# Optimization experiments

Measured on AMD Instinct MI355X. Metric: run time of the kernel, lower is better.

Reference implementation:

```python
import jax, jax.numpy as jnp
import numpy as np

N, K, DIM = 100000, 16, 128


def setup_inputs() -> dict:
    key = jax.random.key(0)
    k1, k2, k3, k4 = jax.random.split(key, 4)
    latents = jax.random.normal(k1, (N, DIM), dtype=jnp.float32)
    neighbors = jax.random.randint(k2, (N, K), 0, N, dtype=jnp.int64)
    # score MLP params: Linear(2*dim -> dim), ReLU, Linear(dim -> 1)
    s1 = 1.0 / np.sqrt(2 * DIM)
    s2 = 1.0 / np.sqrt(DIM)
    W1 = jax.random.uniform(k3, (2 * DIM, DIM), minval=-s1, maxval=s1, dtype=jnp.float32)
    b1 = jnp.zeros((DIM,), dtype=jnp.float32)
    W2 = jax.random.uniform(k4, (DIM, 1), minval=-s2, maxval=s2, dtype=jnp.float32)
    b2 = jnp.zeros((1,), dtype=jnp.float32)
    return {"latents": latents, "neighbors": neighbors, "W1": W1, "b1": b1, "W2": W2, "b2": b2}


def reference(latents, neighbors, W1, b1, W2, b2):
    # latents: [N, D]; neighbors: [N, K] int indices
    nbr = latents[neighbors]                                  # [N, K, D] gather
    central = jnp.broadcast_to(latents[:, None, :], nbr.shape)  # [N, K, D]
    pair = jnp.concatenate([central, nbr], axis=-1)           # [N, K, 2D]
    h = jax.nn.relu(jnp.einsum('nkd,dh->nkh', pair, W1) + b1)  # [N, K, D]
    scores = (jnp.einsum('nkh,ho->nko', h, W2) + b2)[..., 0]   # [N, K]
    weights = jax.nn.softmax(scores, axis=-1)                  # [N, K]
    return jnp.einsum('nk,nkd->nd', weights, nbr)              # [N, D]
```

## Files before the change

kernel.cpp:

```cpp
#include <hip/hip_runtime.h>
#include <hip/hip_bf16.h>

#define DIM 128
#define KNB 16

using fragAB = __attribute__((ext_vector_type(8))) short;
using f32x4  = __attribute__((ext_vector_type(4))) float;
using u32x4  = __attribute__((ext_vector_type(4))) unsigned int;

union frag_u { fragAB s; u32x4 u; };

__device__ __forceinline__ unsigned short bf16bits(float f) {
    union { float f; unsigned u; } v; v.f = f;
    unsigned r = v.u + 0x7fffu + ((v.u >> 16) & 1u);
    return (unsigned short)(r >> 16);
}
__device__ __forceinline__ unsigned cvt_pk_bf16(float lo, float hi) {
    unsigned r;
    asm("v_cvt_pk_bf16_f32 %0, %1, %2" : "=v"(r) : "v"(lo), "v"(hi));
    return r;
}
__device__ __forceinline__ float bflo(unsigned u) { return __uint_as_float(u << 16); }
__device__ __forceinline__ float bfhi(unsigned u) { return __uint_as_float(u & 0xffff0000u); }

__global__ __launch_bounds__(256) void na_w1t(
    const float* __restrict__ W1, const float* __restrict__ W2,
    unsigned short* __restrict__ W1T, unsigned short* __restrict__ W2b)
{
    int idx = blockIdx.x * 256 + threadIdx.x;
    int hp = idx >> 7, d = idx & 127;
    float v = (hp < DIM) ? W1[(size_t)d * DIM + hp]
                         : W1[(size_t)(DIM + d) * DIM + (hp - DIM)];
    W1T[idx] = bf16bits(v);
    if (blockIdx.x == 0 && threadIdx.x < DIM) W2b[threadIdx.x] = bf16bits(W2[threadIdx.x]);
}

__global__ __launch_bounds__(256) void na_precompute_mfma(
    const float* __restrict__ lat, const unsigned short* __restrict__ W1T,
    const float* __restrict__ b1, unsigned short* __restrict__ Ab,
    unsigned short* __restrict__ P, int nNodes)
{
    __shared__ unsigned char w1lds[256 * 256];

    const int wave = threadIdx.x >> 6;
    const int lane = threadIdx.x & 63;
    const int lg = lane >> 4, lr = lane & 15;
    const int mbase = blockIdx.x * 128 + wave * 32;

#pragma unroll
    for (int p = 0; p < 16; ++p) {
        int g = p * 256 + threadIdx.x;
        int row = g >> 4, c = g & 15;
        u32x4 v = *(const u32x4*)(W1T + (size_t)g * 8);
        *(u32x4*)(w1lds + row * 256 + ((c * 16) ^ ((row & 7) << 4))) = v;
    }

    f32x4 acc0[16], acc1[16];
#pragma unroll
    for (int i = 0; i < 16; ++i) {
        acc0[i] = (f32x4){0.f, 0.f, 0.f, 0.f};
        acc1[i] = (f32x4){0.f, 0.f, 0.f, 0.f};
    }

    const int r0 = mbase + lr;
    const int r1 = mbase + 16 + lr;
    const bool v0 = r0 < nNodes, v1 = r1 < nNodes;
    const float* p0 = lat + (size_t)(v0 ? r0 : (nNodes - 1)) * DIM;
    const float* p1 = lat + (size_t)(v1 ? r1 : (nNodes - 1)) * DIM;

    frag_u bl0[4], bl1[4];
#pragma unroll
    for (int ks = 0; ks < 4; ++ks) {
        f32x4 lo0 = *(const f32x4*)(p0 + ks * 32 + lg * 8);
        f32x4 hi0 = *(const f32x4*)(p0 + ks * 32 + lg * 8 + 4);
        f32x4 lo1 = *(const f32x4*)(p1 + ks * 32 + lg * 8);
        f32x4 hi1 = *(const f32x4*)(p1 + ks * 32 + lg * 8 + 4);
        bl0[ks].u[0] = cvt_pk_bf16(lo0[0], lo0[1]);
        bl0[ks].u[1] = cvt_pk_bf16(lo0[2], lo0[3]);
        bl0[ks].u[2] = cvt_pk_bf16(hi0[0], hi0[1]);
        bl0[ks].u[3] = cvt_pk_bf16(hi0[2], hi0[3]);
        bl1[ks].u[0] = cvt_pk_bf16(lo1[0], lo1[1]);
        bl1[ks].u[1] = cvt_pk_bf16(lo1[2], lo1[3]);
        bl1[ks].u[2] = cvt_pk_bf16(hi1[0], hi1[1]);
        bl1[ks].u[3] = cvt_pk_bf16(hi1[2], hi1[3]);
    }

    __syncthreads();

    const unsigned char* wbase = w1lds + lr * 256;
    const int xm = (lr & 7) << 4;
#pragma unroll
    for (int ks = 0; ks < 4; ++ks) {
        const int co = (ks * 64) | (lg * 16);
        const unsigned char* wk = wbase + (co ^ xm);
#pragma unroll
        for (int nt = 0; nt < 16; ++nt) {
            fragAB af = *(const fragAB*)(wk + nt * 4096);
            acc0[nt] = __builtin_amdgcn_mfma_f32_16x16x32_bf16(af, bl0[ks].s, acc0[nt], 0, 0, 0);
            acc1[nt] = __builtin_amdgcn_mfma_f32_16x16x32_bf16(af, bl1[ks].s, acc1[nt], 0, 0, 0);
        }
    }

    if (v0) {
        unsigned short* arow = Ab + (size_t)r0 * DIM;
        unsigned short* prow = P  + (size_t)r0 * 256;
#pragma unroll
        for (int nt = 0; nt < 8; ++nt) {
            float4 bv = *(const float4*)(b1 + nt * 16 + lg * 4);
            uint2 pk;
            pk.x = cvt_pk_bf16(acc0[nt][0] + bv.x, acc0[nt][1] + bv.y);
            pk.y = cvt_pk_bf16(acc0[nt][2] + bv.z, acc0[nt][3] + bv.w);
            *(uint2*)(arow + nt * 16 + lg * 4) = pk;
        }
#pragma unroll
        for (int nt = 8; nt < 16; ++nt) {
            uint2 pk;
            pk.x = cvt_pk_bf16(acc0[nt][0], acc0[nt][1]);
            pk.y = cvt_pk_bf16(acc0[nt][2], acc0[nt][3]);
            *(uint2*)(prow + (nt - 8) * 16 + lg * 4) = pk;
        }
#pragma unroll
        for (int ks = 0; ks < 4; ++ks)
            *(fragAB*)(prow + DIM + ks * 32 + lg * 8) = bl0[ks].s;
    }
    if (v1) {
        unsigned short* arow = Ab + (size_t)r1 * DIM;
        unsigned short* prow = P  + (size_t)r1 * 256;
#pragma unroll
        for (int nt = 0; nt < 8; ++nt) {
            float4 bv = *(const float4*)(b1 + nt * 16 + lg * 4);
            uint2 pk;
            pk.x = cvt_pk_bf16(acc1[nt][0] + bv.x, acc1[nt][1] + bv.y);
            pk.y = cvt_pk_bf16(acc1[nt][2] + bv.z, acc1[nt][3] + bv.w);
            *(uint2*)(arow + nt * 16 + lg * 4) = pk;
        }
#pragma unroll
        for (int nt = 8; nt < 16; ++nt) {
            uint2 pk;
            pk.x = cvt_pk_bf16(acc1[nt][0], acc1[nt][1]);
            pk.y = cvt_pk_bf16(acc1[nt][2], acc1[nt][3]);
            *(uint2*)(prow + (nt - 8) * 16 + lg * 4) = pk;
        }
#pragma unroll
        for (int ks = 0; ks < 4; ++ks)
            *(fragAB*)(prow + DIM + ks * 32 + lg * 8) = bl1[ks].s;
    }
}

__global__ __launch_bounds__(256) void na_score_agg(
    const int* __restrict__ nbr, const unsigned short* __restrict__ Ab,
    const unsigned short* __restrict__ Pu, const unsigned int* __restrict__ P32,
    const unsigned short* __restrict__ W2b, float* __restrict__ out, int nNodes)
{
    const int wave = threadIdx.x >> 6;
    const int lane = threadIdx.x & 63;
    const int lg = lane >> 4, lr = lane & 15;
    const int n = blockIdx.x * 4 + wave;
    if (n >= nNodes) return;

    const int jl = nbr[n * KNB + lr];

    frag_u fB[4];
    const unsigned short* Pj = Pu + (size_t)jl * 256;
#pragma unroll
    for (int ks = 0; ks < 4; ++ks)
        fB[ks].s = *(const fragAB*)(Pj + ks * 32 + lg * 8);

    unsigned bL[KNB];
#pragma unroll
    for (int k = 0; k < KNB; ++k) {
        int j = __shfl(jl, k);
        bL[k] = P32[(size_t)j * 128 + 64 + lane];
    }

    frag_u fA[4]; fragAB fW[4];
    const unsigned short* An = Ab + (size_t)n * DIM;
#pragma unroll
    for (int ks = 0; ks < 4; ++ks) {
        fA[ks].s = *(const fragAB*)(An + ks * 32 + lg * 8);
        fW[ks]   = *(const fragAB*)(W2b + ks * 32 + lg * 8);
    }

    f32x4 accS = (f32x4){0.f, 0.f, 0.f, 0.f};
#pragma unroll
    for (int ks = 0; ks < 4; ++ks) {
        u32x4 alo = fA[ks].u << 16, ahi = fA[ks].u & 0xffff0000u;
        u32x4 blo = fB[ks].u << 16, bhi = fB[ks].u & 0xffff0000u;
        frag_u h;
#pragma unroll
        for (int p = 0; p < 4; ++p) {
            float h0 = fmaxf(__uint_as_float(alo[p]) + __uint_as_float(blo[p]), 0.f);
            float h1 = fmaxf(__uint_as_float(ahi[p]) + __uint_as_float(bhi[p]), 0.f);
            h.u[p] = cvt_pk_bf16(h0, h1);
        }
        accS = __builtin_amdgcn_mfma_f32_16x16x32_bf16(h.s, fW[ks], accS, 0, 0, 0);
    }

    float m = fmaxf(fmaxf(accS[0], accS[1]), fmaxf(accS[2], accS[3]));
    m = fmaxf(m, __shfl_xor(m, 16));
    m = fmaxf(m, __shfl_xor(m, 32));

    float e4[4];
#pragma unroll
    for (int r = 0; r < 4; ++r) e4[r] = __expf(accS[r] - m);

    float sum = e4[0] + e4[1] + e4[2] + e4[3];
    sum += __shfl_xor(sum, 16);
    sum += __shfl_xor(sum, 32);
    const float inv = 1.f / sum;

    const bool hi1 = lg & 1, hi2 = lg & 2;
    float o4[4];
#pragma unroll
    for (int r = 0; r < 4; ++r) o4[r] = __shfl_xor(e4[r], 16);
    float v8[8];
#pragma unroll
    for (int r = 0; r < 4; ++r) {
        v8[r]     = hi1 ? o4[r] : e4[r];
        v8[4 + r] = hi1 ? e4[r] : o4[r];
    }
    float o8[8];
#pragma unroll
    for (int i = 0; i < 8; ++i) o8[i] = __shfl_xor(v8[i], 32);
    float e[KNB];
#pragma unroll
    for (int i = 0; i < 8; ++i) {
        e[i]     = hi2 ? o8[i] : v8[i];
        e[8 + i] = hi2 ? v8[i] : o8[i];
    }

    float o0 = 0.f, o1 = 0.f;
#pragma unroll
    for (int k = 0; k < KNB; ++k) {
        o0 += e[k] * bflo(bL[k]);
        o1 += e[k] * bfhi(bL[k]);
    }

    float2 o; o.x = o0 * inv; o.y = o1 * inv;
    *(float2*)(out + (size_t)n * DIM + 2 * lane) = o;
}

__global__ __launch_bounds__(256) void na_naive(
    const float* __restrict__ lat, const int* __restrict__ nbr,
    const float* __restrict__ W1, const float* __restrict__ b1,
    const float* __restrict__ W2, float* __restrict__ out, int nNodes)
{
    const int wave = threadIdx.x >> 6;
    const int lane = threadIdx.x & 63;
    const int n = blockIdx.x * 4 + wave;
    if (n >= nNodes) return;

    const int d0 = lane, d1 = lane + 64;
    const float w20 = W2[d0];
    const float w21 = W2[d1];
    const float c0 = lat[(size_t)n * DIM + d0];
    const float c1 = lat[(size_t)n * DIM + d1];

    float a0 = b1[d0], a1 = b1[d1];
    for (int r = 0; r < DIM; ++r) {
        float cv = (r < 64) ? __shfl(c0, r) : __shfl(c1, r - 64);
        a0 += cv * W1[(size_t)r * DIM + d0];
        a1 += cv * W1[(size_t)r * DIM + d1];
    }

    const int jl = nbr[n * KNB + (lane & 15)];
    float s[KNB], nl0[KNB], nl1[KNB];

    for (int k = 0; k < KNB; ++k) {
        int j = __shfl(jl, k);
        float l0 = lat[(size_t)j * DIM + d0];
        float l1 = lat[(size_t)j * DIM + d1];
        nl0[k] = l0; nl1[k] = l1;
        float h0 = a0, h1 = a1;
        for (int r = 0; r < DIM; ++r) {
            float nv = (r < 64) ? __shfl(l0, r) : __shfl(l1, r - 64);
            h0 += nv * W1[(size_t)(DIM + r) * DIM + d0];
            h1 += nv * W1[(size_t)(DIM + r) * DIM + d1];
        }
        h0 = fmaxf(h0, 0.f);
        h1 = fmaxf(h1, 0.f);
        float p = h0 * w20 + h1 * w21;
#pragma unroll
        for (int off = 32; off; off >>= 1) p += __shfl_xor(p, off);
        s[k] = p;
    }

    float m = s[0];
#pragma unroll
    for (int k = 1; k < KNB; ++k) m = fmaxf(m, s[k]);
    float sum = 0.f;
#pragma unroll
    for (int k = 0; k < KNB; ++k) { s[k] = expf(s[k] - m); sum += s[k]; }
    float inv = 1.f / sum;

    float o0 = 0.f, o1 = 0.f;
#pragma unroll
    for (int k = 0; k < KNB; ++k) { o0 += s[k] * nl0[k]; o1 += s[k] * nl1[k]; }

    out[(size_t)n * DIM + d0] = o0 * inv;
    out[(size_t)n * DIM + d1] = o1 * inv;
}

extern "C" void kernel_launch(void* const* d_in, const int* in_sizes, int n_in,
                              void* d_out, int out_size, void* d_ws, size_t ws_size,
                              hipStream_t stream)
{
    const float* lat = (const float*)d_in[0];
    const int*   nbr = (const int*)  d_in[1];
    const float* W1  = (const float*)d_in[2];
    const float* b1  = (const float*)d_in[3];
    const float* W2  = (const float*)d_in[4];
    float* out = (float*)d_out;

    const int nNodes = in_sizes[0] / DIM;
    const size_t bytesAb = (size_t)nNodes * DIM * sizeof(unsigned short);
    const size_t bytesP  = (size_t)nNodes * 256 * sizeof(unsigned short);
    const size_t bytesW  = (256 * DIM + DIM) * sizeof(unsigned short);

    if (ws_size >= bytesAb + bytesP + bytesW) {
        unsigned short* Ab  = (unsigned short*)d_ws;
        unsigned short* P   = (unsigned short*)((char*)d_ws + bytesAb);
        unsigned short* W1T = (unsigned short*)((char*)d_ws + bytesAb + bytesP);
        unsigned short* W2b = W1T + 256 * DIM;
        na_w1t<<<128, 256, 0, stream>>>(W1, W2, W1T, W2b);
        na_precompute_mfma<<<(nNodes + 127) / 128, 256, 0, stream>>>(lat, W1T, b1, Ab, P, nNodes);
        na_score_agg<<<(nNodes + 3) / 4, 256, 0, stream>>>(nbr, Ab, P, (const unsigned int*)P, W2b, out, nNodes);
    } else {
        na_naive<<<(nNodes + 3) / 4, 256, 0, stream>>>(lat, nbr, W1, b1, W2, out, nNodes);
    }
}
```

Measured before the change: 162.3 us.

## Recompute neighbor projection per edge via MFMA instead of storing per-node P

The precompute kernel now computes and stores only the central-node projection (with bias) and a bf16 copy of latents, no longer the neighbor projection half of W1. The score kernel loads the neighbor half of W1 into LDS and recomputes each neighbor's projection per edge with MFMA, fusing ReLU and the W2 dot into the epilogue. It processes two nodes per wave in a persistent grid-stride loop. This trades far less precompute writing and a smaller gathered row for 16x more matmul work in the score kernel.

```diff
diff --git a/kernel.cpp b/kernel.cpp
--- a/kernel.cpp
+++ b/kernel.cpp
@@ -38,9 +38,9 @@
 __global__ __launch_bounds__(256) void na_precompute_mfma(
     const float* __restrict__ lat, const unsigned short* __restrict__ W1T,
     const float* __restrict__ b1, unsigned short* __restrict__ Ab,
-    unsigned short* __restrict__ P, int nNodes)
-{
-    __shared__ unsigned char w1lds[256 * 256];
+    unsigned short* __restrict__ latb, int nNodes)
+{
+    __shared__ unsigned char w1lds[128 * 256];
 
     const int wave = threadIdx.x >> 6;
     const int lane = threadIdx.x & 63;
@@ -48,18 +48,11 @@
     const int mbase = blockIdx.x * 128 + wave * 32;
 
 #pragma unroll
-    for (int p = 0; p < 16; ++p) {
+    for (int p = 0; p < 8; ++p) {
         int g = p * 256 + threadIdx.x;
         int row = g >> 4, c = g & 15;
         u32x4 v = *(const u32x4*)(W1T + (size_t)g * 8);
         *(u32x4*)(w1lds + row * 256 + ((c * 16) ^ ((row & 7) << 4))) = v;
-    }
-
-    f32x4 acc0[16], acc1[16];
-#pragma unroll
-    for (int i = 0; i < 16; ++i) {
-        acc0[i] = (f32x4){0.f, 0.f, 0.f, 0.f};
-        acc1[i] = (f32x4){0.f, 0.f, 0.f, 0.f};
     }
 
     const int r0 = mbase + lr;
@@ -87,6 +80,13 @@
 
     __syncthreads();
 
+    f32x4 acc0[8], acc1[8];
+#pragma unroll
+    for (int i = 0; i < 8; ++i) {
+        acc0[i] = (f32x4){0.f, 0.f, 0.f, 0.f};
+        acc1[i] = (f32x4){0.f, 0.f, 0.f, 0.f};
+    }
+
     const unsigned char* wbase = w1lds + lr * 256;
     const int xm = (lr & 7) << 4;
 #pragma unroll
@@ -94,7 +94,7 @@
         const int co = (ks * 64) | (lg * 16);
         const unsigned char* wk = wbase + (co ^ xm);
 #pragma unroll
-        for (int nt = 0; nt < 16; ++nt) {
+        for (int nt = 0; nt < 8; ++nt) {
             fragAB af = *(const fragAB*)(wk + nt * 4096);
             acc0[nt] = __builtin_amdgcn_mfma_f32_16x16x32_bf16(af, bl0[ks].s, acc0[nt], 0, 0, 0);
             acc1[nt] = __builtin_amdgcn_mfma_f32_16x16x32_bf16(af, bl1[ks].s, acc1[nt], 0, 0, 0);
@@ -102,8 +102,8 @@
     }
 
     if (v0) {
-        unsigned short* arow = Ab + (size_t)r0 * DIM;
-        unsigned short* prow = P  + (size_t)r0 * 256;
+        unsigned short* arow = Ab   + (size_t)r0 * DIM;
+        unsigned short* lrow = latb + (size_t)r0 * DIM;
 #pragma unroll
         for (int nt = 0; nt < 8; ++nt) {
             float4 bv = *(const float4*)(b1 + nt * 16 + lg * 4);
@@ -113,19 +113,12 @@
             *(uint2*)(arow + nt * 16 + lg * 4) = pk;
         }
 #pragma unroll
-        for (int nt = 8; nt < 16; ++nt) {
-            uint2 pk;
-            pk.x = cvt_pk_bf16(acc0[nt][0], acc0[nt][1]);
-            pk.y = cvt_pk_bf16(acc0[nt][2], acc0[nt][3]);
-            *(uint2*)(prow + (nt - 8) * 16 + lg * 4) = pk;
-        }
-#pragma unroll
         for (int ks = 0; ks < 4; ++ks)
-            *(fragAB*)(prow + DIM + ks * 32 + lg * 8) = bl0[ks].s;
+            *(fragAB*)(lrow + ks * 32 + lg * 8) = bl0[ks].s;
     }
     if (v1) {
-        unsigned short* arow = Ab + (size_t)r1 * DIM;
-        unsigned short* prow = P  + (size_t)r1 * 256;
+        unsigned short* arow = Ab   + (size_t)r1 * DIM;
+        unsigned short* lrow = latb + (size_t)r1 * DIM;
 #pragma unroll
         for (int nt = 0; nt < 8; ++nt) {
             float4 bv = *(const float4*)(b1 + nt * 16 + lg * 4);
@@ -135,109 +128,121 @@
             *(uint2*)(arow + nt * 16 + lg * 4) = pk;
         }
 #pragma unroll
-        for (int nt = 8; nt < 16; ++nt) {
-            uint2 pk;
-            pk.x = cvt_pk_bf16(acc1[nt][0], acc1[nt][1]);
-            pk.y = cvt_pk_bf16(acc1[nt][2], acc1[nt][3]);
-            *(uint2*)(prow + (nt - 8) * 16 + lg * 4) = pk;
-        }
-#pragma unroll
         for (int ks = 0; ks < 4; ++ks)
-            *(fragAB*)(prow + DIM + ks * 32 + lg * 8) = bl1[ks].s;
+            *(fragAB*)(lrow + ks * 32 + lg * 8) = bl1[ks].s;
     }
 }
 
 __global__ __launch_bounds__(256) void na_score_agg(
     const int* __restrict__ nbr, const unsigned short* __restrict__ Ab,
-    const unsigned short* __restrict__ Pu, const unsigned int* __restrict__ P32,
-    const unsigned short* __restrict__ W2b, float* __restrict__ out, int nNodes)
-{
+    const unsigned short* __restrict__ latb, const unsigned int* __restrict__ latb32,
+    const unsigned short* __restrict__ W1T, const unsigned short* __restrict__ W2b,
+    float* __restrict__ out, int nNodes)
+{
+    __shared__ unsigned char w1lds[128 * 256];
+
     const int wave = threadIdx.x >> 6;
     const int lane = threadIdx.x & 63;
     const int lg = lane >> 4, lr = lane & 15;
-    const int n = blockIdx.x * 4 + wave;
-    if (n >= nNodes) return;
-
-    const int jl = nbr[n * KNB + lr];
-
-    frag_u fB[4];
-    const unsigned short* Pj = Pu + (size_t)jl * 256;
-#pragma unroll
-    for (int ks = 0; ks < 4; ++ks)
-        fB[ks].s = *(const fragAB*)(Pj + ks * 32 + lg * 8);
-
-    unsigned bL[KNB];
-#pragma unroll
-    for (int k = 0; k < KNB; ++k) {
-        int j = __shfl(jl, k);
-        bL[k] = P32[(size_t)j * 128 + 64 + lane];
-    }
-
-    frag_u fA[4]; fragAB fW[4];
-    const unsigned short* An = Ab + (size_t)n * DIM;
-#pragma unroll
-    for (int ks = 0; ks < 4; ++ks) {
-        fA[ks].s = *(const fragAB*)(An + ks * 32 + lg * 8);
-        fW[ks]   = *(const fragAB*)(W2b + ks * 32 + lg * 8);
-    }
-
-    f32x4 accS = (f32x4){0.f, 0.f, 0.f, 0.f};
-#pragma unroll
-    for (int ks = 0; ks < 4; ++ks) {
-        u32x4 alo = fA[ks].u << 16, ahi = fA[ks].u & 0xffff0000u;
-        u32x4 blo = fB[ks].u << 16, bhi = fB[ks].u & 0xffff0000u;
-        frag_u h;
-#pragma unroll
-        for (int p = 0; p < 4; ++p) {
-            float h0 = fmaxf(__uint_as_float(alo[p]) + __uint_as_float(blo[p]), 0.f);
-            float h1 = fmaxf(__uint_as_float(ahi[p]) + __uint_as_float(bhi[p]), 0.f);
-            h.u[p] = cvt_pk_bf16(h0, h1);
-        }
-        accS = __builtin_amdgcn_mfma_f32_16x16x32_bf16(h.s, fW[ks], accS, 0, 0, 0);
-    }
-
-    float m = fmaxf(fmaxf(accS[0], accS[1]), fmaxf(accS[2], accS[3]));
-    m = fmaxf(m, __shfl_xor(m, 16));
-    m = fmaxf(m, __shfl_xor(m, 32));
-
-    float e4[4];
-#pragma unroll
-    for (int r = 0; r < 4; ++r) e4[r] = __expf(accS[r] - m);
-
-    float sum = e4[0] + e4[1] + e4[2] + e4[3];
-    sum += __shfl_xor(sum, 16);
-    sum += __shfl_xor(sum, 32);
-    const float inv = 1.f / sum;
-
-    const bool hi1 = lg & 1, hi2 = lg & 2;
-    float o4[4];
-#pragma unroll
-    for (int r = 0; r < 4; ++r) o4[r] = __shfl_xor(e4[r], 16);
-    float v8[8];
-#pragma unroll
-    for (int r = 0; r < 4; ++r) {
-        v8[r]     = hi1 ? o4[r] : e4[r];
-        v8[4 + r] = hi1 ? e4[r] : o4[r];
-    }
-    float o8[8];
-#pragma unroll
-    for (int i = 0; i < 8; ++i) o8[i] = __shfl_xor(v8[i], 32);
-    float e[KNB];
-#pragma unroll
-    for (int i = 0; i < 8; ++i) {
-        e[i]     = hi2 ? o8[i] : v8[i];
-        e[8 + i] = hi2 ? v8[i] : o8[i];
-    }
-
-    float o0 = 0.f, o1 = 0.f;
-#pragma unroll
-    for (int k = 0; k < KNB; ++k) {
-        o0 += e[k] * bflo(bL[k]);
-        o1 += e[k] * bfhi(bL[k]);
-    }
-
-    float2 o; o.x = o0 * inv; o.y = o1 * inv;
-    *(float2*)(out + (size_t)n * DIM + 2 * lane) = o;
+
+#pragma unroll
+    for (int p = 0; p < 8; ++p) {
+        int g = p * 256 + threadIdx.x;
+        int row = g >> 4, c = g & 15;
+        u32x4 v = *(const u32x4*)(W1T + (size_t)(128 + row) * DIM + c * 8);
+        *(u32x4*)(w1lds + row * 256 + ((c * 16) ^ ((row & 7) << 4))) = v;
+    }
+    __syncthreads();
+
+    const unsigned char* wbase = w1lds + lr * 256;
+    const int xm = (lr & 7) << 4;
+    const int nPairs = (nNodes + 1) >> 1;
+
+    for (int pr = blockIdx.x * 4 + wave; pr < nPairs; pr += gridDim.x * 4) {
+        const int n0 = 2 * pr;
+        const int n1 = n0 + 1;
+        const bool has1 = n1 < nNodes;
+        const int n1c = has1 ? n1 : n0;
+
+        const int jl0 = nbr[n0  * KNB + lr];
+        const int jl1 = nbr[n1c * KNB + lr];
+
+        frag_u fL0[4], fL1[4];
+        const unsigned short* L0 = latb + (size_t)jl0 * DIM;
+        const unsigned short* L1 = latb + (size_t)jl1 * DIM;
+#pragma unroll
+        for (int ks = 0; ks < 4; ++ks) {
+            fL0[ks].s = *(const fragAB*)(L0 + ks * 32 + lg * 8);
+            fL1[ks].s = *(const fragAB*)(L1 + ks * 32 + lg * 8);
+        }
+
+        float sacc0 = 0.f, sacc1 = 0.f;
+        const unsigned short* An0 = Ab + (size_t)n0  * DIM;
+        const unsigned short* An1 = Ab + (size_t)n1c * DIM;
+#pragma unroll
+        for (int nt = 0; nt < 8; ++nt) {
+            f32x4 acc0 = (f32x4){0.f, 0.f, 0.f, 0.f};
+            f32x4 acc1 = (f32x4){0.f, 0.f, 0.f, 0.f};
+#pragma unroll
+            for (int ks = 0; ks < 4; ++ks) {
+                const int co = (ks * 64) | (lg * 16);
+                fragAB af = *(const fragAB*)(wbase + nt * 4096 + (co ^ xm));
+                acc0 = __builtin_amdgcn_mfma_f32_16x16x32_bf16(af, fL0[ks].s, acc0, 0, 0, 0);
+                acc1 = __builtin_amdgcn_mfma_f32_16x16x32_bf16(af, fL1[ks].s, acc1, 0, 0, 0);
+            }
+            uint2 a0 = *(const uint2*)(An0 + nt * 16 + lg * 4);
+            uint2 a1 = *(const uint2*)(An1 + nt * 16 + lg * 4);
+            uint2 wv = *(const uint2*)(W2b + nt * 16 + lg * 4);
+            float w0 = bflo(wv.x), w1 = bfhi(wv.x), w2 = bflo(wv.y), w3 = bfhi(wv.y);
+            sacc0 += fmaxf(bflo(a0.x) + acc0[0], 0.f) * w0
+                   + fmaxf(bfhi(a0.x) + acc0[1], 0.f) * w1
+                   + fmaxf(bflo(a0.y) + acc0[2], 0.f) * w2
+                   + fmaxf(bfhi(a0.y) + acc0[3], 0.f) * w3;
+            sacc1 += fmaxf(bflo(a1.x) + acc1[0], 0.f) * w0
+                   + fmaxf(bfhi(a1.x) + acc1[1], 0.f) * w1
+                   + fmaxf(bflo(a1.y) + acc1[2], 0.f) * w2
+                   + fmaxf(bfhi(a1.y) + acc1[3], 0.f) * w3;
+        }
+        float s0 = sacc0 + __shfl_xor(sacc0, 16);
+        s0 += __shfl_xor(s0, 32);
+        float s1 = sacc1 + __shfl_xor(sacc1, 16);
+        s1 += __shfl_xor(s1, 32);
+
+        float m0 = s0, m1 = s1;
+#pragma unroll
+        for (int off = 1; off < 16; off <<= 1) {
+            m0 = fmaxf(m0, __shfl_xor(m0, off));
+            m1 = fmaxf(m1, __shfl_xor(m1, off));
+        }
+        float e0 = __expf(s0 - m0);
+        float e1 = __expf(s1 - m1);
+        float sum0 = e0, sum1 = e1;
+#pragma unroll
+        for (int off = 1; off < 16; off <<= 1) {
+            sum0 += __shfl_xor(sum0, off);
+            sum1 += __shfl_xor(sum1, off);
+        }
+        const float inv0 = 1.f / sum0;
+        const float inv1 = 1.f / sum1;
+
+        float o00 = 0.f, o01 = 0.f, o10 = 0.f, o11 = 0.f;
+#pragma unroll
+        for (int k = 0; k < KNB; ++k) {
+            int j0 = __shfl(jl0, k); float ek0 = __shfl(e0, k);
+            int j1 = __shfl(jl1, k); float ek1 = __shfl(e1, k);
+            unsigned u0 = latb32[(size_t)j0 * 64 + lane];
+            unsigned u1 = latb32[(size_t)j1 * 64 + lane];
+            o00 += ek0 * bflo(u0); o01 += ek0 * bfhi(u0);
+            o10 += ek1 * bflo(u1); o11 += ek1 * bfhi(u1);
+        }
+
+        float2 r0; r0.x = o00 * inv0; r0.y = o01 * inv0;
+        *(float2*)(out + (size_t)n0 * DIM + 2 * lane) = r0;
+        if (has1) {
+            float2 r1; r1.x = o10 * inv1; r1.y = o11 * inv1;
+            *(float2*)(out + (size_t)n1 * DIM + 2 * lane) = r1;
+        }
+    }
 }
 
 __global__ __launch_bounds__(256) void na_naive(
@@ -314,17 +319,18 @@
 
     const int nNodes = in_sizes[0] / DIM;
     const size_t bytesAb = (size_t)nNodes * DIM * sizeof(unsigned short);
-    const size_t bytesP  = (size_t)nNodes * 256 * sizeof(unsigned short);
+    const size_t bytesL  = (size_t)nNodes * DIM * sizeof(unsigned short);
     const size_t bytesW  = (256 * DIM + DIM) * sizeof(unsigned short);
 
-    if (ws_size >= bytesAb + bytesP + bytesW) {
-        unsigned short* Ab  = (unsigned short*)d_ws;
-        unsigned short* P   = (unsigned short*)((char*)d_ws + bytesAb);
-        unsigned short* W1T = (unsigned short*)((char*)d_ws + bytesAb + bytesP);
-        unsigned short* W2b = W1T + 256 * DIM;
+    if (ws_size >= bytesAb + bytesL + bytesW) {
+        unsigned short* Ab   = (unsigned short*)d_ws;
+        unsigned short* latb = (unsigned short*)((char*)d_ws + bytesAb);
+        unsigned short* W1T  = (unsigned short*)((char*)d_ws + bytesAb + bytesL);
+        unsigned short* W2b  = W1T + 256 * DIM;
         na_w1t<<<128, 256, 0, stream>>>(W1, W2, W1T, W2b);
-        na_precompute_mfma<<<(nNodes + 127) / 128, 256, 0, stream>>>(lat, W1T, b1, Ab, P, nNodes);
-        na_score_agg<<<(nNodes + 3) / 4, 256, 0, stream>>>(nbr, Ab, P, (const unsigned int*)P, W2b, out, nNodes);
+        na_precompute_mfma<<<(nNodes + 127) / 128, 256, 0, stream>>>(lat, W1T, b1, Ab, latb, nNodes);
+        na_score_agg<<<1280, 256, 0, stream>>>(nbr, Ab, latb, (const unsigned int*)latb,
+                                               W1T, W2b, out, nNodes);
     } else {
         na_naive<<<(nNodes + 3) / 4, 256, 0, stream>>>(lat, nbr, W1, b1, W2, out, nNodes);
     }
```

New measurement: 297.7 us. 83.4% more time.
